# Performance work log

Measured on AMD Instinct MI355X. Metric: run time of the kernel, lower is better.

## Reference

```python
import jax, jax.numpy as jnp
import numpy as np

H, D = 8, 16
HID = H * D  # hidden_channels = 128
SQRT_D = float(np.sqrt(D))


def setup_inputs() -> dict:
    key = jax.random.key(0)
    ks = iter(jax.random.split(key, 64))
    def nrm(shape, scale):
        return jax.random.normal(next(ks), shape, dtype=jnp.float32) * scale
    def rint(n, hi):
        return jax.random.randint(next(ks), (n,), 0, hi, dtype=jnp.int32)
    E = 250000
    Nh, Ni, Nt = 8000, 40000, 20000
    inp = {
        'x_herb': nrm((Nh, 400), 1.0),
        'x_ing':  nrm((Ni, 300), 1.0),
        'x_tgt':  nrm((Nt, 200), 1.0),
        # per-type input projections
        'W_herb': nrm((400, HID), 0.05), 'b_herb': jnp.zeros((HID,), jnp.float32),
        'W_ing':  nrm((300, HID), 0.06), 'b_ing':  jnp.zeros((HID,), jnp.float32),
        'W_tgt':  nrm((200, HID), 0.07), 'b_tgt':  jnp.zeros((HID,), jnp.float32),
        # HGTConv per-node-type k/q/v linears, stacked over [herb, ing, tgt]
        'Wk': nrm((3, HID, HID), 0.09), 'bk': jnp.zeros((3, HID), jnp.float32),
        'Wq': nrm((3, HID, HID), 0.09), 'bq': jnp.zeros((3, HID), jnp.float32),
        'Wv': nrm((3, HID, HID), 0.09), 'bv': jnp.zeros((3, HID), jnp.float32),
        # per-edge-type relation matrices / priors, stacked over 4 edge types
        'a_rel': nrm((4, H, D, D), 0.25),
        'm_rel': nrm((4, H, D, D), 0.25),
        'p_rel': jnp.ones((4, H), jnp.float32),
        # per-dst-node-type output linear + skip gate
        'Wa': nrm((3, HID, HID), 0.09), 'ba': jnp.zeros((3, HID), jnp.float32),
        'skip': jnp.ones((3,), jnp.float32),
        # final herb linear
        'W_out': nrm((HID, HID), 0.09), 'b_out': jnp.zeros((HID,), jnp.float32),
        # edge lists: (herb->ing contains), (ing->herb rev), (ing->tgt targets), (tgt->ing rev)
        'src_ci': rint(E, Nh), 'dst_ci': rint(E, Ni),
        'src_ic': rint(E, Ni), 'dst_ic': rint(E, Nh),
        'src_it': rint(E, Ni), 'dst_it': rint(E, Nt),
        'src_ti': rint(E, Nt), 'dst_ti': rint(E, Ni),
    }
    return inp


def _hetero_forward(x_herb, x_ing, x_tgt, W_herb, b_herb, W_ing, b_ing, W_tgt, b_tgt,
                    Wk, bk, Wq, bq, Wv, bv, a_rel, m_rel, p_rel, Wa, ba, skip,
                    W_out, b_out, src_ci, dst_ci, src_ic, dst_ic, src_it, dst_it,
                    src_ti, dst_ti):
    types = ['herb', 'ing', 'tgt']
    xs = {'herb': x_herb @ W_herb + b_herb,
          'ing':  x_ing  @ W_ing  + b_ing,
          'tgt':  x_tgt  @ W_tgt  + b_tgt}
    Ns = {t: xs[t].shape[0] for t in types}
    # per-node-type k/q/v, reshaped to [N, H, D]
    k = {t: (xs[t] @ Wk[i] + bk[i]).reshape(-1, H, D) for i, t in enumerate(types)}
    q = {t: (xs[t] @ Wq[i] + bq[i]).reshape(-1, H, D) for i, t in enumerate(types)}
    v = {t: (xs[t] @ Wv[i] + bv[i]).reshape(-1, H, D) for i, t in enumerate(types)}

    edge_defs = [  # (edge_type_id, src_type, dst_type, src_idx, dst_idx)
        (0, 'herb', 'ing', src_ci, dst_ci),
        (1, 'ing', 'herb', src_ic, dst_ic),
        (2, 'ing', 'tgt', src_it, dst_it),
        (3, 'tgt', 'ing', src_ti, dst_ti),
    ]
    contrib = {t: [] for t in types}
    for e, s, t, src, dst in edge_defs:
        # relation-specific transforms at node level, then gather per edge
        k_rel = jnp.einsum('nhd,hde->nhe', k[s], a_rel[e])  # [Ns, H, D]
        v_rel = jnp.einsum('nhd,hde->nhe', v[s], m_rel[e])  # [Ns, H, D]
        logit = (q[t][dst] * k_rel[src]).sum(-1) * (p_rel[e] / SQRT_D)  # [E, H]
        contrib[t].append((logit, v_rel[src], dst))

    out = {}
    for i, t in enumerate(types):
        logits = jnp.concatenate([c[0] for c in contrib[t]], axis=0)  # [Et, H]
        msgs = jnp.concatenate([c[1] for c in contrib[t]], axis=0)    # [Et, H, D]
        dsts = jnp.concatenate([c[2] for c in contrib[t]], axis=0)    # [Et]
        n = Ns[t]
        # segment softmax over all incoming edges of each dst node (per head)
        mx = jax.ops.segment_max(logits, dsts, num_segments=n)
        ex = jnp.exp(logits - mx[dsts])
        den = jax.ops.segment_sum(ex, dsts, num_segments=n)
        alpha = ex / (den[dsts] + 1e-16)
        agg = jax.ops.segment_sum(msgs * alpha[:, :, None], dsts, num_segments=n)
        agg = agg.reshape(n, HID)
        o = jax.nn.gelu(agg, approximate=False) @ Wa[i] + ba[i]
        g = jax.nn.sigmoid(skip[i])
        out[t] = jax.nn.relu(g * o + (1.0 - g) * xs[t])
    out_herb = out['herb'] @ W_out + b_out
    return (out_herb, out['ing'], out['tgt'])


def reference(x_herb, x_ing, x_tgt, W_herb, b_herb, W_ing, b_ing, W_tgt, b_tgt,
              Wk, bk, Wq, bq, Wv, bv, a_rel, m_rel, p_rel, Wa, ba, skip,
              W_out, b_out, src_ci, dst_ci, src_ic, dst_ic, src_it, dst_it,
              src_ti, dst_ti):
    return _hetero_forward(x_herb, x_ing, x_tgt, W_herb, b_herb, W_ing, b_ing,
                           W_tgt, b_tgt, Wk, bk, Wq, bq, Wv, bv, a_rel, m_rel,
                           p_rel, Wa, ba, skip, W_out, b_out, src_ci, dst_ci,
                           src_ic, dst_ic, src_it, dst_it, src_ti, dst_ti)
```

## Files before the change

### kernel.cpp

```cpp
#include <hip/hip_runtime.h>
#include <math.h>

#define HID 128
typedef unsigned int uint;
typedef unsigned short ushort;
typedef __attribute__((ext_vector_type(8))) short short8;
typedef __attribute__((ext_vector_type(4))) float floatx4;
typedef __attribute__((ext_vector_type(2))) float f32x2;

__device__ __forceinline__ ushort f2b(float f) {
  uint u = __float_as_uint(f);
  u += 0x7fffu + ((u >> 16) & 1u);
  return (ushort)(u >> 16);
}
__device__ __forceinline__ float b2f(ushort s) {
  return __uint_as_float(((uint)s) << 16);
}
__device__ __forceinline__ float blo(uint u) { return __uint_as_float(u << 16); }
__device__ __forceinline__ float bhi(uint u) { return __uint_as_float(u & 0xffff0000u); }
__device__ __forceinline__ f32x2 b2x2(uint u) {
  f32x2 r;
  r.x = __uint_as_float(u << 16);
  r.y = __uint_as_float(u & 0xffff0000u);
  return r;
}

__device__ __forceinline__ void gll16(const ushort* g, ushort* l) {
  __builtin_amdgcn_global_load_lds(
      (const __attribute__((address_space(1))) void*)g,
      (__attribute__((address_space(3))) void*)l, 16, 0, 0);
}

__device__ __forceinline__ size_t a_packed_us(int rr, int col) {
  int tm = rr >> 7, prow = rr & 127;
  int ptk = col >> 5, kin = col & 31;
  int sw = (kin >> 3) ^ ((prow >> 1) & 3);
  return (((size_t)tm * 4 + ptk) * 512 + (size_t)prow * 4 + sw) * 8 + (kin & 7);
}

#define CSR_CH 2048
#define CSR_SH 9

struct EdgeStreams {
  const int* src[4]; const int* dst[4];
  int off[4]; uint rel[4]; uint ldb[4];
};

struct PackSeg { const float* X; ushort* out; int M, K, Ktiles, start; };
struct WBlk { const float* src; ushort* dst; int K; int start; };
struct Prolog {
  PackSeg pk[3];
  int crwstart, wstart, bstart, total;
  const float *Wk, *bk, *Wv, *bv, *a_rel, *m_rel, *p_rel;
  ushort* kw_dst[4];
  ushort* vw_dst[4];
  float* bcat;
  int kb_off[4], vb_off[4];
  WBlk wb[10];
  const float* bq;
  int bq_off[3];
  const int* edst[4];
  int eoff[4];
  uint* hist;
  int NBs, NBH, NBK, E;
};

__device__ void combine_rel_elem(const Prolog& P, int idx)
{
  int col  = idx & 127;
  int rest = idx >> 7;
  int row  = rest % 129;
  rest /= 129;
  int kv = rest & 1;
  int e  = rest >> 1;
  int i  = (e + 1) >> 1;
  int h = col >> 4, j = col & 15;
  const float* Wsrc = kv ? P.Wv : P.Wk;
  const float* bsrc = kv ? P.bv : P.bk;
  const float* rel  = kv ? P.m_rel : P.a_rel;
  float acc = 0.f;
  if (row < 128) {
#pragma unroll
    for (int d = 0; d < 16; ++d)
      acc += Wsrc[(size_t)i * 16384 + (size_t)row * 128 + h * 16 + d] *
             rel[((e * 8 + h) * 16 + d) * 16 + j];
  } else {
#pragma unroll
    for (int d = 0; d < 16; ++d)
      acc += bsrc[i * 128 + h * 16 + d] * rel[((e * 8 + h) * 16 + d) * 16 + j];
  }
  if (!kv) acc *= P.p_rel[e * 8 + h] * 0.36067376022224085f;
  if (row < 128) {
    ushort* dst = kv ? P.vw_dst[e] : P.kw_dst[e];
    int tk = row >> 5, chunk = (row >> 3) & 3, m = row & 7;
    int swf = chunk ^ ((col >> 1) & 3);
    dst[((tk * 512 + col * 4 + swf) << 3) + m] = f2b(acc);
  } else {
    P.bcat[(kv ? P.vb_off[e] : P.kb_off[e]) + col] = acc;
  }
}

__device__ void conv_elem(const Prolog& P, int s0)
{
  int si = 0;
#pragma unroll
  for (int k = 1; k < 10; ++k)
    if (s0 >= P.wb[k].start) si = k;
  WBlk b = P.wb[si];
  int s = s0 - b.start;
  int tk = s >> 9, o = s & 511;
  int c = o >> 2, swf = o & 3;
  int chunk = swf ^ ((c >> 1) & 3);
  int r0 = tk * 32 + chunk * 8;
  ushort tmp[8];
#pragma unroll
  for (int m = 0; m < 8; ++m) {
    int r = r0 + m;
    tmp[m] = (r < b.K) ? f2b(b.src[(size_t)r * 128 + c]) : (ushort)0;
  }
  *(short8*)&b.dst[(size_t)s * 8] = *(short8*)tmp;
}

__global__ __launch_bounds__(256)
void prologue(Prolog P)
{
  __shared__ uint h[512];
  int bI = blockIdx.x;
  if (bI < P.NBH) {
    int et = bI / P.NBs;
    int i0 = (bI - et * P.NBs) * CSR_CH;
    const int* dp = P.edst[et];
    int off = P.eoff[et];
    for (int t = threadIdx.x; t < P.NBK; t += 256) h[t] = 0;
    __syncthreads();
#pragma unroll
    for (int j = 0; j < CSR_CH / 256; ++j) {
      int idx = i0 + j * 256 + threadIdx.x;
      if (idx < P.E) atomicAdd(&h[(uint)(off + dp[idx]) >> CSR_SH], 1u);
    }
    __syncthreads();
    for (int t = threadIdx.x; t < P.NBK; t += 256)
      P.hist[(size_t)t * P.NBH + bI] = h[t];
    return;
  }
  int gtid = (bI - P.NBH) * 256 + threadIdx.x;
  if (gtid >= P.total) return;
  if (gtid >= P.bstart) {
    int j = gtid - P.bstart;
    P.bcat[P.bq_off[j >> 7] + (j & 127)] = P.bq[j];
    return;
  }
  if (gtid >= P.wstart) { conv_elem(P, gtid - P.wstart); return; }
  if (gtid >= P.crwstart) { combine_rel_elem(P, gtid - P.crwstart); return; }
  int si = 0;
  if (gtid >= P.pk[2].start) si = 2;
  else if (gtid >= P.pk[1].start) si = 1;
  const PackSeg s = P.pk[si];
  int slot = gtid - s.start;
  int spm = s.Ktiles << 9;
  int tm = slot / spm, r2 = slot - tm * spm;
  int tk = r2 >> 9, o = r2 & 511;
  int row = o >> 2, sw = o & 3;
  int chunk = sw ^ ((row >> 1) & 3);
  int grow = tm * 128 + row;
  int gk = tk * 32 + chunk * 8;
  ushort tmp[8];
  if (grow < s.M && gk + 8 <= s.K) {
    const float* p = s.X + (size_t)grow * s.K + gk;
    float4 a = *(const float4*)p, b = *(const float4*)(p + 4);
    tmp[0] = f2b(a.x); tmp[1] = f2b(a.y); tmp[2] = f2b(a.z); tmp[3] = f2b(a.w);
    tmp[4] = f2b(b.x); tmp[5] = f2b(b.y); tmp[6] = f2b(b.z); tmp[7] = f2b(b.w);
  } else {
#pragma unroll
    for (int j = 0; j < 8; ++j) {
      int kk = gk + j;
      tmp[j] = (grow < s.M && kk < s.K) ? f2b(s.X[(size_t)grow * s.K + kk]) : (ushort)0;
    }
  }
  *(short8*)&s.out[(size_t)slot * 8] = *(short8*)tmp;
}

__global__ __launch_bounds__(256)
void bucket_scan(uint* __restrict__ hist, uint* __restrict__ bucketTot, int NBH)
{
  __shared__ uint ws[4];
  __shared__ uint carry_s;
  int b = blockIdx.x;
  int t = threadIdx.x, lane = t & 63, w = t >> 6;
  if (t == 0) carry_s = 0;
  __syncthreads();
  for (int base = 0; base < NBH; base += 256) {
    int i = base + t;
    uint x = (i < NBH) ? hist[(size_t)b * NBH + i] : 0u;
    uint v = x;
#pragma unroll
    for (int o = 1; o < 64; o <<= 1) {
      uint y = __shfl_up(v, o, 64);
      if (lane >= o) v += y;
    }
    if (lane == 63) ws[w] = v;
    __syncthreads();
    uint add = carry_s;
    for (int k = 0; k < w; ++k) add += ws[k];
    if (i < NBH) hist[(size_t)b * NBH + i] = add + v - x;
    __syncthreads();
    if (t == 255) carry_s = add + v;
    __syncthreads();
  }
  if (t == 0) bucketTot[b] = carry_s;
}

__device__ __forceinline__ void base_scan(const uint* __restrict__ bucketTot,
                                          uint* sb, uint* ws, int NBK)
{
  int t = threadIdx.x, lane = t & 63, w = t >> 6;
  sb[t] = (t < NBK) ? bucketTot[t] : 0u;
  sb[t + 256] = (t + 256 < NBK) ? bucketTot[t + 256] : 0u;
  __syncthreads();
  uint a0 = sb[2 * t], a1 = sb[2 * t + 1];
  uint s = a0 + a1;
  uint v = s;
#pragma unroll
  for (int o = 1; o < 64; o <<= 1) {
    uint y = __shfl_up(v, o, 64);
    if (lane >= o) v += y;
  }
  if (lane == 63) ws[w] = v;
  __syncthreads();
  uint add = 0;
  for (int k = 0; k < w; ++k) add += ws[k];
  uint e0 = add + v - s;
  sb[2 * t] = e0;
  sb[2 * t + 1] = e0 + a0;
  __syncthreads();
}

__global__ __launch_bounds__(256)
void bucket_scatter(EdgeStreams es, const uint* __restrict__ hist,
                    const uint* __restrict__ bucketTot,
                    uint2* __restrict__ inter, int NBs, int NBH, int NBK, int E)
{
  __shared__ uint sb[516];
  __shared__ uint ws[4];
  __shared__ uint cur[512];
  base_scan(bucketTot, sb, ws, NBK);
  int b = blockIdx.x;
  int et = b / NBs;
  int i0 = (b - et * NBs) * CSR_CH;
  const int* dp = es.dst[et];
  const int* sp = es.src[et];
  int off = es.off[et];
  uint rel = es.rel[et], ldb = es.ldb[et];
  for (int t = threadIdx.x; t < NBK; t += 256)
    cur[t] = sb[t] + hist[(size_t)t * NBH + b];
  __syncthreads();
#pragma unroll
  for (int j = 0; j < CSR_CH / 256; ++j) {
    int idx = i0 + j * 256 + threadIdx.x;
    if (idx < E) {
      int g = off + dp[idx];
      uint pos = atomicAdd(&cur[(uint)g >> CSR_SH], 1u);
      inter[pos] = make_uint2(rel + (uint)sp[idx] * ldb, (uint)g);
    }
  }
}

__global__ __launch_bounds__(256)
void bucket_finalize(const uint2* __restrict__ inter,
                     const uint* __restrict__ bucketTot,
                     int* __restrict__ starts, uint* __restrict__ payload,
                     int Ntot, int NBK)
{
  __shared__ uint sb[516];
  __shared__ uint ncnt[512];
  __shared__ uint ws[4];
  base_scan(bucketTot, sb, ws, NBK);
  int b = blockIdx.x;
  int g0 = b << CSR_SH;
  int t = threadIdx.x, lane = t & 63, w = t >> 6;
  uint r0 = sb[b], r1 = sb[b + 1];
  if (b == NBK - 1 && t == 0) starts[Ntot] = (int)r1;
  ncnt[t] = 0; ncnt[t + 256] = 0;
  __syncthreads();
  for (uint i = r0 + t; i < r1; i += 256)
    atomicAdd(&ncnt[inter[i].y - g0], 1u);
  __syncthreads();
  uint a0 = ncnt[2 * t], a1 = ncnt[2 * t + 1];
  uint s = a0 + a1;
  uint v = s;
#pragma unroll
  for (int o = 1; o < 64; o <<= 1) {
    uint y = __shfl_up(v, o, 64);
    if (lane >= o) v += y;
  }
  if (lane == 63) ws[w] = v;
  __syncthreads();
  uint add = r0;
  for (int k = 0; k < w; ++k) add += ws[k];
  uint e0 = add + v - s;
  int gi = g0 + 2 * t;
  if (gi < Ntot)     starts[gi]     = (int)e0;
  if (gi + 1 < Ntot) starts[gi + 1] = (int)(e0 + a0);
  ncnt[2 * t] = e0;
  ncnt[2 * t + 1] = e0 + a0;
  __syncthreads();
  for (uint i = r0 + t; i < r1; i += 256) {
    uint2 rec = inter[i];
    uint pos = atomicAdd(&ncnt[rec.y - g0], 1u);
    payload[pos] = rec.x;
  }
}

struct GemmSeg {
  const ushort* A; const ushort* B; const float* bias;
  void* out; const ushort* xsP;
  int Ktiles, ldo, Mreal, skip_idx, epi, NT, start;
  int n2; const ushort* B2; const float* bias2;
  void* out2; int ldo2, Mreal2, epi2;
};
struct Gemm3 { GemmSeg s[3]; const float* skip; int nseg; };

__launch_bounds__(256)
__global__ void gemm_sched(Gemm3 g3)
{
  __shared__ __align__(16) ushort As[2][4096];
  __shared__ __align__(16) ushort Bs[2][4096];
  __shared__ __align__(16) ushort Xs[16384];
  int bid = blockIdx.x;
  int si = 0;
  if (g3.nseg > 1 && bid >= g3.s[1].start)
    si = (g3.nseg > 2 && bid >= g3.s[2].start) ? 2 : 1;
  const GemmSeg sg = g3.s[si];
  int local = bid - sg.start;
  int tm = local / sg.NT, tn = local - tm * sg.NT;

  const int t = threadIdx.x;
  const int wave = t >> 6, lane = t & 63;
  const int wm = (wave >> 1) * 64, wn = (wave & 1) * 64;
  const int l16 = lane & 15, quad = lane >> 4;
  const int Ktiles = sg.Ktiles;
  const int swz = (quad ^ ((l16 >> 1) & 3)) * 8;

  const ushort* Abase = sg.A + (size_t)tm * Ktiles * 4096;
  const ushort* Bbase = sg.B + (size_t)tn * Ktiles * 4096;

  floatx4 acc[4][4];
#pragma unroll
  for (int i = 0; i < 4; ++i)
#pragma unroll
    for (int j = 0; j < 4; ++j) acc[i][j] = (floatx4){0.f, 0.f, 0.f, 0.f};

  auto stage = [&](int tk, int buf) {
#pragma unroll
    for (int j = 0; j < 4; ++j) {
      int c = wave * 4 + j;
      if (c < 8)
        gll16(Abase + (size_t)tk * 4096 + c * 512 + lane * 8, &As[buf][c * 512]);
      else
        gll16(Bbase + (size_t)tk * 4096 + (c - 8) * 512 + lane * 8, &Bs[buf][(c - 8) * 512]);
    }
  };

  stage(0, 0);
  __syncthreads();

  for (int tk = 0; tk < Ktiles; ++tk) {
    int buf = tk & 1;
    if (tk + 1 < Ktiles) stage(tk + 1, buf ^ 1);

    short8 af[4], bfr[4];
#pragma unroll
    for (int i = 0; i < 4; ++i) {
      af[i]  = *(const short8*)&As[buf][(wm + i * 16 + l16) * 32 + swz];
      bfr[i] = *(const short8*)&Bs[buf][(wn + i * 16 + l16) * 32 + swz];
    }
#pragma unroll
    for (int mi = 0; mi < 4; ++mi)
#pragma unroll
      for (int ni = 0; ni < 4; ++ni)
        acc[mi][ni] = __builtin_amdgcn_mfma_f32_16x16x32_bf16(
            af[mi], bfr[ni], acc[mi][ni], 0, 0, 0);
    __syncthreads();
  }

  const int epi = sg.epi;
  float g = 0.f, omg = 0.f;
  if (epi == 2 || epi == 3 || epi == 5) {
    float s = g3.skip[sg.skip_idx];
    g = 1.f / (1.f + __expf(-s));
    omg = 1.f - g;
  }
#pragma unroll
  for (int ni = 0; ni < 4; ++ni) {
    int col = tn * 128 + wn + ni * 16 + l16;
    float bb = sg.bias[col];
    int ptk = col >> 5, kin = col & 31;
#pragma unroll
    for (int mi = 0; mi < 4; ++mi) {
      int rloc = wm + mi * 16 + quad * 4;
#pragma unroll
      for (int r = 0; r < 4; ++r) {
        int prow = rloc + r;
        int rr = tm * 128 + prow;
        float v = acc[mi][ni][r] + bb;
        if (epi == 0) {
          ((ushort*)sg.out)[(size_t)rr * sg.ldo + col] = f2b(v);
        } else if (epi == 1) {
          if (rr < sg.Mreal) ((float*)sg.out)[(size_t)rr * sg.ldo + col] = v;
        } else if (epi == 2) {
          if (rr < sg.Mreal) {
            float xo = b2f(sg.xsP[a_packed_us(rr, col)]);
            ((float*)sg.out)[(size_t)rr * sg.ldo + col] = fmaxf(g * v + omg * xo, 0.f);
          }
        } else if (epi == 3) {
          float xo = b2f(sg.xsP[a_packed_us(rr, col)]);
          ((ushort*)sg.out)[a_packed_us(rr, col)] = f2b(fmaxf(g * v + omg * xo, 0.f));
        } else if (epi == 4) {
          ushort bv = f2b(v);
          ((ushort*)sg.out)[a_packed_us(rr, col)] = bv;
          int sw2 = (kin >> 3) ^ ((prow >> 1) & 3);
          Xs[ptk * 4096 + prow * 32 + sw2 * 8 + (kin & 7)] = bv;
        } else {
          float xo = b2f(sg.xsP[a_packed_us(rr, col)]);
          int sw2 = (kin >> 3) ^ ((prow >> 1) & 3);
          Xs[ptk * 4096 + prow * 32 + sw2 * 8 + (kin & 7)] =
              f2b(fmaxf(g * v + omg * xo, 0.f));
        }
      }
    }
  }

  if (sg.n2 == 0) return;
  __syncthreads();
  for (int t2 = 0; t2 < sg.n2; ++t2) {
    const ushort* B2b = sg.B2 + (size_t)t2 * 16384;
    auto stage2 = [&](int tk, int buf) {
#pragma unroll
      for (int j = 0; j < 2; ++j) {
        int c = wave * 2 + j;
        gll16(B2b + (size_t)tk * 4096 + c * 512 + lane * 8, &Bs[buf][c * 512]);
      }
    };
    floatx4 a2[4][4];
#pragma unroll
    for (int i = 0; i < 4; ++i)
#pragma unroll
      for (int j = 0; j < 4; ++j) a2[i][j] = (floatx4){0.f, 0.f, 0.f, 0.f};
    stage2(0, 0);
    __syncthreads();
#pragma unroll
    for (int tk = 0; tk < 4; ++tk) {
      int buf = tk & 1;
      if (tk + 1 < 4) stage2(tk + 1, buf ^ 1);
      short8 af[4], bfr[4];
#pragma unroll
      for (int i = 0; i < 4; ++i) {
        af[i]  = *(const short8*)&Xs[tk * 4096 + (wm + i * 16 + l16) * 32 + swz];
        bfr[i] = *(const short8*)&Bs[buf][(wn + i * 16 + l16) * 32 + swz];
      }
#pragma unroll
      for (int mi = 0; mi < 4; ++mi)
#pragma unroll
        for (int ni = 0; ni < 4; ++ni)
          a2[mi][ni] = __builtin_amdgcn_mfma_f32_16x16x32_bf16(
              af[mi], bfr[ni], a2[mi][ni], 0, 0, 0);
      __syncthreads();
    }
#pragma unroll
    for (int ni = 0; ni < 4; ++ni) {
      int col = t2 * 128 + wn + ni * 16 + l16;
      float bb = sg.bias2[col];
#pragma unroll
      for (int mi = 0; mi < 4; ++mi) {
        int rloc = wm + mi * 16 + quad * 4;
#pragma unroll
        for (int r = 0; r < 4; ++r) {
          int rr = tm * 128 + rloc + r;
          float v = a2[mi][ni][r] + bb;
          if (sg.epi2 == 0) {
            ((ushort*)sg.out2)[(size_t)rr * sg.ldo2 + col] = f2b(v);
          } else {
            if (rr < sg.Mreal2) ((float*)sg.out2)[(size_t)rr * sg.ldo2 + col] = v;
          }
        }
      }
    }
  }
}

struct GatherType { const ushort* q; ushort* agg; int ldq; };
struct GatherDesc { GatherType ty[3]; int n0, n1; };

__launch_bounds__(256)
__global__ void gather_all(const int* __restrict__ starts,
                           const uint* __restrict__ payload,
                           const ushort* __restrict__ kvbase,
                           GatherDesc gd, int Ntot)
{
  int wid = (blockIdx.x * 256 + threadIdx.x) >> 6;
  if (wid >= Ntot) return;
  int lane = threadIdx.x & 63;
  int g = lane >> 4, l = lane & 15;

  GatherType T;
  int d;
  if (wid < gd.n0)      { T = gd.ty[0]; d = wid; }
  else if (wid < gd.n1) { T = gd.ty[1]; d = wid - gd.n0; }
  else                  { T = gd.ty[2]; d = wid - gd.n1; }

  const char* kvb = (const char*)kvbase;
  const uint lofs = (uint)l * 16u;

  uint4 qv = *(const uint4*)(T.q + (size_t)d * T.ldq + l * 8);
  f32x2 q0 = b2x2(qv.x), q1 = b2x2(qv.y), q2 = b2x2(qv.z), q3 = b2x2(qv.w);

  int e0 = starts[wid], e1 = starts[wid + 1];
  float lsum = 0.f;
  f32x2 ac0 = {0.f, 0.f}, ac1 = {0.f, 0.f}, ac2 = {0.f, 0.f}, ac3 = {0.f, 0.f};

  for (int eb = e0; eb < e1; eb += 8) {
    int eA = eb + g, eB = eA + 4;
    bool actA = eA < e1, actB = eB < e1;
    uint pA = payload[actA ? eA : e0];
    uint pB = payload[actB ? eB : e0];
    const char* bA = kvb + (pA + lofs);
    const char* bB = kvb + (pB + lofs);
    uint4 kA = *(const uint4*)bA;
    uint4 vA = *(const uint4*)(bA + 256);
    uint4 kB = *(const uint4*)bB;
    uint4 vB = *(const uint4*)(bB + 256);

    f32x2 dA = q0 * b2x2(kA.x);
    dA = __builtin_elementwise_fma(q1, b2x2(kA.y), dA);
    dA = __builtin_elementwise_fma(q2, b2x2(kA.z), dA);
    dA = __builtin_elementwise_fma(q3, b2x2(kA.w), dA);
    f32x2 dB = q0 * b2x2(kB.x);
    dB = __builtin_elementwise_fma(q1, b2x2(kB.y), dB);
    dB = __builtin_elementwise_fma(q2, b2x2(kB.z), dB);
    dB = __builtin_elementwise_fma(q3, b2x2(kB.w), dB);
    float pa = dA.x + dA.y;
    float pb = dB.x + dB.y;
    pa += __shfl_xor(pa, 1, 64);
    pb += __shfl_xor(pb, 1, 64);
    float exA = exp2f(fminf(pa, 115.4f));
    float exB = exp2f(fminf(pb, 115.4f));
    exA = actA ? exA : 0.f;
    exB = actB ? exB : 0.f;
    lsum += exA + exB;
    f32x2 xA = {exA, exA}, xB = {exB, exB};
    ac0 = __builtin_elementwise_fma(xA, b2x2(vA.x), ac0);
    ac1 = __builtin_elementwise_fma(xA, b2x2(vA.y), ac1);
    ac2 = __builtin_elementwise_fma(xA, b2x2(vA.z), ac2);
    ac3 = __builtin_elementwise_fma(xA, b2x2(vA.w), ac3);
    ac0 = __builtin_elementwise_fma(xB, b2x2(vB.x), ac0);
    ac1 = __builtin_elementwise_fma(xB, b2x2(vB.y), ac1);
    ac2 = __builtin_elementwise_fma(xB, b2x2(vB.z), ac2);
    ac3 = __builtin_elementwise_fma(xB, b2x2(vB.w), ac3);
  }

  float s0 = ac0.x, s1 = ac0.y, s2 = ac1.x, s3 = ac1.y;
  float s4 = ac2.x, s5 = ac2.y, s6 = ac3.x, s7 = ac3.y;
#define MRG(v) v += __shfl_xor(v, 16, 64); v += __shfl_xor(v, 32, 64)
  MRG(lsum); MRG(s0); MRG(s1); MRG(s2); MRG(s3); MRG(s4); MRG(s5); MRG(s6); MRG(s7);
#undef MRG

  float inv = 1.f / (lsum + 1e-16f);
  float m0 = (g & 1) ? s2 : s0, m1 = (g & 1) ? s6 : s4;
  float n0 = (g & 1) ? s3 : s1, n1 = (g & 1) ? s7 : s5;
  float x0 = ((g & 2) ? m1 : m0) * inv;
  float x1 = ((g & 2) ? n1 : n0) * inv;
  float g0 = 0.5f * x0 * (1.f + erff(x0 * 0.70710678118654752f));
  float g1 = 0.5f * x1 * (1.f + erff(x1 * 0.70710678118654752f));
  int tm = d >> 7, row = d & 127;
  int tk = l >> 2, sw = (l & 3) ^ ((row >> 1) & 3);
  size_t us = (((size_t)tm * 4 + tk) * 512 + (size_t)row * 4 + sw) * 8 + 2 * g;
  *(uint*)(T.agg + us) = ((uint)f2b(g1) << 16) | (uint)f2b(g0);
}

extern "C" void kernel_launch(void* const* d_in, const int* in_sizes, int n_in,
                              void* d_out, int out_size, void* d_ws, size_t ws_size,
                              hipStream_t stream)
{
  const float* x_herb = (const float*)d_in[0];
  const float* x_ing  = (const float*)d_in[1];
  const float* x_tgt  = (const float*)d_in[2];
  const float* W_herb = (const float*)d_in[3];
  const float* b_herb = (const float*)d_in[4];
  const float* W_ing  = (const float*)d_in[5];
  const float* b_ing  = (const float*)d_in[6];
  const float* W_tgt  = (const float*)d_in[7];
  const float* b_tgt  = (const float*)d_in[8];
  const float* Wk     = (const float*)d_in[9];
  const float* bk     = (const float*)d_in[10];
  const float* Wq     = (const float*)d_in[11];
  const float* bq     = (const float*)d_in[12];
  const float* Wv     = (const float*)d_in[13];
  const float* bv     = (const float*)d_in[14];
  const float* a_rel  = (const float*)d_in[15];
  const float* m_rel  = (const float*)d_in[16];
  const float* p_rel  = (const float*)d_in[17];
  const float* Wa     = (const float*)d_in[18];
  const float* ba     = (const float*)d_in[19];
  const float* skip   = (const float*)d_in[20];
  const float* W_out  = (const float*)d_in[21];
  const float* b_out  = (const float*)d_in[22];
  const int* srcs[4] = {(const int*)d_in[23], (const int*)d_in[25],
                        (const int*)d_in[27], (const int*)d_in[29]};
  const int* dsts[4] = {(const int*)d_in[24], (const int*)d_in[26],
                        (const int*)d_in[28], (const int*)d_in[30]};

  const int Nh = in_sizes[0] / 400;
  const int Ni = in_sizes[1] / 300;
  const int Nt = in_sizes[2] / 200;
  const int E  = in_sizes[23];
  const int Ntot = Nh + Ni + Nt;

  const int MT_h = (Nh + 127) / 128, MT_i = (Ni + 127) / 128, MT_t = (Nt + 127) / 128;
  const int KT_h = 13, KT_i = 10, KT_t = 7;

  const int NBs = (E + CSR_CH - 1) / CSR_CH;
  const int NBH = 4 * NBs;
  const int NBK = (Ntot + (1 << CSR_SH) - 1) >> CSR_SH;

  char* base = (char*)d_ws;
  size_t off = 0;
  auto A = [&](size_t bytes) -> void* {
    void* p = base + off; off += (bytes + 255) & ~(size_t)255; return p;
  };
  ushort* xp_h  = (ushort*)A((size_t)MT_h * KT_h * 8192);
  ushort* xp_i  = (ushort*)A((size_t)MT_i * KT_i * 8192);
  ushort* xp_t  = (ushort*)A((size_t)MT_t * KT_t * 8192);
  ushort* xsP_h = (ushort*)A((size_t)MT_h * 4 * 8192);
  ushort* xsP_i = (ushort*)A((size_t)MT_i * 4 * 8192);
  ushort* xsP_t = (ushort*)A((size_t)MT_t * 4 * 8192);
  ushort* fused_h = (ushort*)A((size_t)MT_h * 128 * 384 * 2);
  ushort* fused_i = (ushort*)A((size_t)MT_i * 128 * 640 * 2);
  ushort* fused_t = (ushort*)A((size_t)MT_t * 128 * 384 * 2);
  ushort* aggp_h  = (ushort*)A((size_t)MT_h * 4 * 8192);
  ushort* aggp_i  = (ushort*)A((size_t)MT_i * 4 * 8192);
  ushort* aggp_t  = (ushort*)A((size_t)MT_t * 4 * 8192);
  ushort* Weff1_h = (ushort*)A((size_t)KT_h * 8192);
  ushort* Weff1_i = (ushort*)A((size_t)KT_i * 8192);
  ushort* Weff1_t = (ushort*)A((size_t)KT_t * 8192);
  ushort* Wcat_h = (ushort*)A((size_t)3 * 4 * 8192);
  ushort* Wcat_i = (ushort*)A((size_t)5 * 4 * 8192);
  ushort* Wcat_t = (ushort*)A((size_t)3 * 4 * 8192);
  float* bcat   = (float*)A(1408 * 4);
  ushort* Wa_t   = (ushort*)A((size_t)3 * 16384 * 2);
  ushort* Wout_t = (ushort*)A((size_t)16384 * 2);
  int* starts  = (int*)A((size_t)(Ntot + 4) * 4);
  uint* payload = (uint*)A((size_t)(4 * E + 8) * 4);
  uint* hist    = (uint*)A((size_t)NBK * NBH * 4);
  uint* bucketTot  = (uint*)A((size_t)NBK * 4);
  uint2* inter  = (uint2*)A((size_t)(4 * E + 8) * 8);
  (void)ws_size; (void)n_in;

  const int toff_h = 0, toff_i = Nh, toff_t = Nh + Ni;
  dim3 blk(256);

  uint fi2 = (uint)((size_t)(fused_i - fused_h) * 2);
  uint ft2 = (uint)((size_t)(fused_t - fused_h) * 2);

  int sl_h = MT_h * KT_h * 512, sl_i = MT_i * KT_i * 512, sl_t = MT_t * KT_t * 512;
  Prolog P;
  P.pk[0] = {x_herb, xp_h, Nh, 400, KT_h, 0};
  P.pk[1] = {x_ing,  xp_i, Ni, 300, KT_i, sl_h};
  P.pk[2] = {x_tgt,  xp_t, Nt, 200, KT_t, sl_h + sl_i};
  P.crwstart = sl_h + sl_i + sl_t;
  P.wstart = P.crwstart + 4 * 2 * 129 * 128;
  {
    const float* wsrc10[10] = {W_herb, W_ing, W_tgt, Wq, Wq + 16384, Wq + 32768,
                               Wa, Wa + 16384, Wa + 32768, W_out};
    ushort* wdst10[10] = {Weff1_h, Weff1_i, Weff1_t, Wcat_h, Wcat_i, Wcat_t,
                          Wa_t, Wa_t + 16384, Wa_t + 32768, Wout_t};
    int wk10[10] = {400, 300, 200, 128, 128, 128, 128, 128, 128, 128};
    int wcum = 0;
    for (int z = 0; z < 10; ++z) {
      P.wb[z] = {wsrc10[z], wdst10[z], wk10[z], wcum};
      wcum += ((wk10[z] + 31) / 32) * 512;
    }
    P.bstart = P.wstart + wcum;
  }
  P.total = P.bstart + 384;
  P.Wk = Wk; P.bk = bk; P.Wv = Wv; P.bv = bv;
  P.a_rel = a_rel; P.m_rel = m_rel; P.p_rel = p_rel;
  P.kw_dst[0] = Wcat_h + 16384; P.vw_dst[0] = Wcat_h + 32768;
  P.kw_dst[1] = Wcat_i + 16384; P.vw_dst[1] = Wcat_i + 32768;
  P.kw_dst[2] = Wcat_i + 49152; P.vw_dst[2] = Wcat_i + 65536;
  P.kw_dst[3] = Wcat_t + 16384; P.vw_dst[3] = Wcat_t + 32768;
  P.bcat = bcat;
  P.kb_off[0] = 128;  P.vb_off[0] = 256;
  P.kb_off[1] = 512;  P.vb_off[1] = 640;
  P.kb_off[2] = 768;  P.vb_off[2] = 896;
  P.kb_off[3] = 1152; P.vb_off[3] = 1280;
  P.bq = bq;
  P.bq_off[0] = 0; P.bq_off[1] = 384; P.bq_off[2] = 1024;
  P.edst[0] = dsts[0]; P.eoff[0] = toff_i;
  P.edst[1] = dsts[1]; P.eoff[1] = toff_h;
  P.edst[2] = dsts[2]; P.eoff[2] = toff_t;
  P.edst[3] = dsts[3]; P.eoff[3] = toff_i;
  P.hist = hist; P.NBs = NBs; P.NBH = NBH; P.NBK = NBK; P.E = E;
  prologue<<<NBH + (P.total + 255) / 256, blk, 0, stream>>>(P);

  EdgeStreams ES;
  ES.src[0] = srcs[0]; ES.dst[0] = dsts[0]; ES.off[0] = toff_i;
  ES.rel[0] = 256u;        ES.ldb[0] = 768u;
  ES.src[1] = srcs[1]; ES.dst[1] = dsts[1]; ES.off[1] = toff_h;
  ES.rel[1] = fi2 + 256u;  ES.ldb[1] = 1280u;
  ES.src[2] = srcs[2]; ES.dst[2] = dsts[2]; ES.off[2] = toff_t;
  ES.rel[2] = fi2 + 768u;  ES.ldb[2] = 1280u;
  ES.src[3] = srcs[3]; ES.dst[3] = dsts[3]; ES.off[3] = toff_i;
  ES.rel[3] = ft2 + 256u;  ES.ldb[3] = 768u;
  bucket_scan<<<NBK, blk, 0, stream>>>(hist, bucketTot, NBH);
  bucket_scatter<<<NBH, blk, 0, stream>>>(ES, hist, bucketTot, inter, NBs, NBH, NBK, E);
  bucket_finalize<<<NBK, blk, 0, stream>>>(inter, bucketTot, starts, payload, Ntot, NBK);

  Gemm3 G1;
  G1.skip = skip; G1.nseg = 3;
  G1.s[0] = {xp_h, Weff1_h, b_herb, xsP_h, nullptr, KT_h, 0, 0, 0, 4, 1, 0,
             3, Wcat_h, bcat + 0, fused_h, 384, 0, 0};
  G1.s[1] = {xp_i, Weff1_i, b_ing,  xsP_i, nullptr, KT_i, 0, 0, 0, 4, 1, MT_h,
             5, Wcat_i, bcat + 384, fused_i, 640, 0, 0};
  G1.s[2] = {xp_t, Weff1_t, b_tgt,  xsP_t, nullptr, KT_t, 0, 0, 0, 4, 1, MT_h + MT_i,
             3, Wcat_t, bcat + 1024, fused_t, 384, 0, 0};
  gemm_sched<<<MT_h + MT_i + MT_t, blk, 0, stream>>>(G1);

  GatherDesc GD;
  GD.n0 = Nh; GD.n1 = Nh + Ni;
  GD.ty[0] = {fused_h, aggp_h, 384};
  GD.ty[1] = {fused_i, aggp_i, 640};
  GD.ty[2] = {fused_t, aggp_t, 384};
  gather_all<<<(Ntot + 3) / 4, blk, 0, stream>>>(starts, payload, fused_h, GD, Ntot);

  float* outp = (float*)d_out;
  float* out_herb = outp;
  float* out_ing  = outp + (size_t)Nh * HID;
  float* out_tgt  = outp + (size_t)(Nh + Ni) * HID;
  Gemm3 GE;
  GE.skip = skip; GE.nseg = 3;
  GE.s[0] = {aggp_h, Wa_t + 0 * 16384, ba + 0 * 128, nullptr, xsP_h,
             4, 0, 0, 0, 5, 1, 0,
             1, Wout_t, b_out, out_herb, 128, Nh, 1};
  GE.s[1] = {aggp_i, Wa_t + 1 * 16384, ba + 1 * 128, out_ing, xsP_i,
             4, 128, Ni, 1, 2, 1, MT_h,
             0, nullptr, nullptr, nullptr, 0, 0, 0};
  GE.s[2] = {aggp_t, Wa_t + 2 * 16384, ba + 2 * 128, out_tgt, xsP_t,
             4, 128, Nt, 2, 2, 1, MT_h + MT_i,
             0, nullptr, nullptr, nullptr, 0, 0, 0};
  gemm_sched<<<MT_h + MT_i + MT_t, blk, 0, stream>>>(GE);
  (void)out_size;
}
```

Measured before the change: 436.7 us.

## Alias GEMM LDS buffers, swap MFMA operands for vectorized epilogue stores

Merges the As/Bs/Xs shared arrays into a single aliased LDS region, cutting the GEMM kernel's shared memory footprint so more blocks can fit per CU. Swaps the MFMA operand order so each lane holds four consecutive output columns, which lets the epilogue use float4 bias loads and uint2/float4 vector stores in place of scalar stores. The second fused GEMM is restructured into a single continuous pipelined loop over all N2 tiles. Its first B2 tile is now prefetched before the first epilogue runs. Aliasing Xs onto the A/B staging buffers depends on correct barrier placement, and the prefetched B2 region must not overlap Xs.

Result: faster. 399.1 us (-8.6%).

```diff
diff --git a/kernel.cpp b/kernel.cpp
--- a/kernel.cpp
+++ b/kernel.cpp
@@ -323,9 +323,12 @@
 __launch_bounds__(256)
 __global__ void gemm_sched(Gemm3 g3)
 {
-  __shared__ __align__(16) ushort As[2][4096];
-  __shared__ __align__(16) ushort Bs[2][4096];
-  __shared__ __align__(16) ushort Xs[16384];
+  __shared__ __align__(16) ushort lds[24576];
+  ushort* As0 = lds;
+  ushort* Bs0 = lds + 8192;
+  ushort* Xs  = lds;
+  ushort* B2s = lds + 16384;
+
   int bid = blockIdx.x;
   int si = 0;
   if (g3.nseg > 1 && bid >= g3.s[1].start)
@@ -355,9 +358,17 @@
     for (int j = 0; j < 4; ++j) {
       int c = wave * 4 + j;
       if (c < 8)
-        gll16(Abase + (size_t)tk * 4096 + c * 512 + lane * 8, &As[buf][c * 512]);
+        gll16(Abase + (size_t)tk * 4096 + c * 512 + lane * 8, As0 + buf * 4096 + c * 512);
       else
-        gll16(Bbase + (size_t)tk * 4096 + (c - 8) * 512 + lane * 8, &Bs[buf][(c - 8) * 512]);
+        gll16(Bbase + (size_t)tk * 4096 + (c - 8) * 512 + lane * 8,
+              Bs0 + buf * 4096 + (c - 8) * 512);
+    }
+  };
+  auto stage2L = [&](int s2, int buf) {
+#pragma unroll
+    for (int j = 0; j < 2; ++j) {
+      int c = wave * 2 + j;
+      gll16(sg.B2 + (size_t)s2 * 4096 + c * 512 + lane * 8, B2s + buf * 4096 + c * 512);
     }
   };
 
@@ -371,17 +382,19 @@
     short8 af[4], bfr[4];
 #pragma unroll
     for (int i = 0; i < 4; ++i) {
-      af[i]  = *(const short8*)&As[buf][(wm + i * 16 + l16) * 32 + swz];
-      bfr[i] = *(const short8*)&Bs[buf][(wn + i * 16 + l16) * 32 + swz];
+      af[i]  = *(const short8*)&As0[buf * 4096 + (wm + i * 16 + l16) * 32 + swz];
+      bfr[i] = *(const short8*)&Bs0[buf * 4096 + (wn + i * 16 + l16) * 32 + swz];
     }
 #pragma unroll
     for (int mi = 0; mi < 4; ++mi)
 #pragma unroll
       for (int ni = 0; ni < 4; ++ni)
         acc[mi][ni] = __builtin_amdgcn_mfma_f32_16x16x32_bf16(
-            af[mi], bfr[ni], acc[mi][ni], 0, 0, 0);
+            bfr[ni], af[mi], acc[mi][ni], 0, 0, 0);
     __syncthreads();
   }
+
+  if (sg.n2 > 0) stage2L(0, 0);
 
   const int epi = sg.epi;
   float g = 0.f, omg = 0.f;
@@ -392,96 +405,110 @@
   }
 #pragma unroll
   for (int ni = 0; ni < 4; ++ni) {
-    int col = tn * 128 + wn + ni * 16 + l16;
-    float bb = sg.bias[col];
-    int ptk = col >> 5, kin = col & 31;
+    int cl = wn + ni * 16 + quad * 4;
+    int cb = tn * 128 + cl;
+    float4 b4 = *(const float4*)&sg.bias[cb];
 #pragma unroll
     for (int mi = 0; mi < 4; ++mi) {
-      int rloc = wm + mi * 16 + quad * 4;
-#pragma unroll
-      for (int r = 0; r < 4; ++r) {
-        int prow = rloc + r;
-        int rr = tm * 128 + prow;
-        float v = acc[mi][ni][r] + bb;
-        if (epi == 0) {
-          ((ushort*)sg.out)[(size_t)rr * sg.ldo + col] = f2b(v);
-        } else if (epi == 1) {
-          if (rr < sg.Mreal) ((float*)sg.out)[(size_t)rr * sg.ldo + col] = v;
-        } else if (epi == 2) {
-          if (rr < sg.Mreal) {
-            float xo = b2f(sg.xsP[a_packed_us(rr, col)]);
-            ((float*)sg.out)[(size_t)rr * sg.ldo + col] = fmaxf(g * v + omg * xo, 0.f);
+      int prow = wm + mi * 16 + l16;
+      int rr = tm * 128 + prow;
+      float v0 = acc[mi][ni][0] + b4.x;
+      float v1 = acc[mi][ni][1] + b4.y;
+      float v2 = acc[mi][ni][2] + b4.z;
+      float v3 = acc[mi][ni][3] + b4.w;
+      if (epi == 0) {
+        uint2 o = make_uint2(((uint)f2b(v1) << 16) | f2b(v0),
+                             ((uint)f2b(v3) << 16) | f2b(v2));
+        *(uint2*)&((ushort*)sg.out)[(size_t)rr * sg.ldo + cb] = o;
+      } else if (epi == 1) {
+        if (rr < sg.Mreal)
+          *(float4*)&((float*)sg.out)[(size_t)rr * sg.ldo + cb] =
+              make_float4(v0, v1, v2, v3);
+      } else if (epi == 2) {
+        if (rr < sg.Mreal) {
+          uint2 xo = *(const uint2*)&sg.xsP[a_packed_us(rr, cb)];
+          float4 o;
+          o.x = fmaxf(g * v0 + omg * blo(xo.x), 0.f);
+          o.y = fmaxf(g * v1 + omg * bhi(xo.x), 0.f);
+          o.z = fmaxf(g * v2 + omg * blo(xo.y), 0.f);
+          o.w = fmaxf(g * v3 + omg * bhi(xo.y), 0.f);
+          *(float4*)&((float*)sg.out)[(size_t)rr * sg.ldo + cb] = o;
+        }
+      } else if (epi == 3) {
+        uint2 xo = *(const uint2*)&sg.xsP[a_packed_us(rr, cb)];
+        uint2 o = make_uint2(
+            ((uint)f2b(fmaxf(g * v1 + omg * bhi(xo.x), 0.f)) << 16) |
+                   f2b(fmaxf(g * v0 + omg * blo(xo.x), 0.f)),
+            ((uint)f2b(fmaxf(g * v3 + omg * bhi(xo.y), 0.f)) << 16) |
+                   f2b(fmaxf(g * v2 + omg * blo(xo.y), 0.f)));
+        *(uint2*)&((ushort*)sg.out)[a_packed_us(rr, cb)] = o;
+      } else if (epi == 4) {
+        uint2 o = make_uint2(((uint)f2b(v1) << 16) | f2b(v0),
+                             ((uint)f2b(v3) << 16) | f2b(v2));
+        *(uint2*)&((ushort*)sg.out)[a_packed_us(rr, cb)] = o;
+        int sw2 = ((cl & 31) >> 3) ^ ((prow >> 1) & 3);
+        *(uint2*)&Xs[(cl >> 5) * 4096 + prow * 32 + sw2 * 8 + (cl & 7)] = o;
+      } else {
+        uint2 xo = *(const uint2*)&sg.xsP[a_packed_us(rr, cb)];
+        uint2 o = make_uint2(
+            ((uint)f2b(fmaxf(g * v1 + omg * bhi(xo.x), 0.f)) << 16) |
+                   f2b(fmaxf(g * v0 + omg * blo(xo.x), 0.f)),
+            ((uint)f2b(fmaxf(g * v3 + omg * bhi(xo.y), 0.f)) << 16) |
+                   f2b(fmaxf(g * v2 + omg * blo(xo.y), 0.f)));
+        int sw2 = ((cl & 31) >> 3) ^ ((prow >> 1) & 3);
+        *(uint2*)&Xs[(cl >> 5) * 4096 + prow * 32 + sw2 * 8 + (cl & 7)] = o;
+      }
+    }
+  }
+
+  if (sg.n2 == 0) return;
+  __syncthreads();
+  int total2 = sg.n2 * 4;
+  floatx4 a2[4][4];
+#pragma unroll
+  for (int i = 0; i < 4; ++i)
+#pragma unroll
+    for (int j = 0; j < 4; ++j) a2[i][j] = (floatx4){0.f, 0.f, 0.f, 0.f};
+  for (int s2 = 0; s2 < total2; ++s2) {
+    int buf = s2 & 1;
+    if (s2 + 1 < total2) stage2L(s2 + 1, buf ^ 1);
+    int xb = (s2 & 3) * 4096;
+    short8 af[4], bfr[4];
+#pragma unroll
+    for (int i = 0; i < 4; ++i) {
+      af[i]  = *(const short8*)&Xs[xb + (wm + i * 16 + l16) * 32 + swz];
+      bfr[i] = *(const short8*)&B2s[buf * 4096 + (wn + i * 16 + l16) * 32 + swz];
+    }
+#pragma unroll
+    for (int mi = 0; mi < 4; ++mi)
+#pragma unroll
+      for (int ni = 0; ni < 4; ++ni)
+        a2[mi][ni] = __builtin_amdgcn_mfma_f32_16x16x32_bf16(
+            bfr[ni], af[mi], a2[mi][ni], 0, 0, 0);
+    __syncthreads();
+    if ((s2 & 3) == 3) {
+      int t2 = s2 >> 2;
+#pragma unroll
+      for (int ni = 0; ni < 4; ++ni) {
+        int cb2 = t2 * 128 + wn + ni * 16 + quad * 4;
+        float4 b4 = *(const float4*)&sg.bias2[cb2];
+#pragma unroll
+        for (int mi = 0; mi < 4; ++mi) {
+          int rr = tm * 128 + wm + mi * 16 + l16;
+          float v0 = a2[mi][ni][0] + b4.x;
+          float v1 = a2[mi][ni][1] + b4.y;
+          float v2 = a2[mi][ni][2] + b4.z;
+          float v3 = a2[mi][ni][3] + b4.w;
+          if (sg.epi2 == 0) {
+            uint2 o = make_uint2(((uint)f2b(v1) << 16) | f2b(v0),
+                                 ((uint)f2b(v3) << 16) | f2b(v2));
+            *(uint2*)&((ushort*)sg.out2)[(size_t)rr * sg.ldo2 + cb2] = o;
+          } else {
+            if (rr < sg.Mreal2)
+              *(float4*)&((float*)sg.out2)[(size_t)rr * sg.ldo2 + cb2] =
+                  make_float4(v0, v1, v2, v3);
           }
-        } else if (epi == 3) {
-          float xo = b2f(sg.xsP[a_packed_us(rr, col)]);
-          ((ushort*)sg.out)[a_packed_us(rr, col)] = f2b(fmaxf(g * v + omg * xo, 0.f));
-        } else if (epi == 4) {
-          ushort bv = f2b(v);
-          ((ushort*)sg.out)[a_packed_us(rr, col)] = bv;
-          int sw2 = (kin >> 3) ^ ((prow >> 1) & 3);
-          Xs[ptk * 4096 + prow * 32 + sw2 * 8 + (kin & 7)] = bv;
-        } else {
-          float xo = b2f(sg.xsP[a_packed_us(rr, col)]);
-          int sw2 = (kin >> 3) ^ ((prow >> 1) & 3);
-          Xs[ptk * 4096 + prow * 32 + sw2 * 8 + (kin & 7)] =
-              f2b(fmaxf(g * v + omg * xo, 0.f));
-        }
-      }
-    }
-  }
-
-  if (sg.n2 == 0) return;
-  __syncthreads();
-  for (int t2 = 0; t2 < sg.n2; ++t2) {
-    const ushort* B2b = sg.B2 + (size_t)t2 * 16384;
-    auto stage2 = [&](int tk, int buf) {
-#pragma unroll
-      for (int j = 0; j < 2; ++j) {
-        int c = wave * 2 + j;
-        gll16(B2b + (size_t)tk * 4096 + c * 512 + lane * 8, &Bs[buf][c * 512]);
-      }
-    };
-    floatx4 a2[4][4];
-#pragma unroll
-    for (int i = 0; i < 4; ++i)
-#pragma unroll
-      for (int j = 0; j < 4; ++j) a2[i][j] = (floatx4){0.f, 0.f, 0.f, 0.f};
-    stage2(0, 0);
-    __syncthreads();
-#pragma unroll
-    for (int tk = 0; tk < 4; ++tk) {
-      int buf = tk & 1;
-      if (tk + 1 < 4) stage2(tk + 1, buf ^ 1);
-      short8 af[4], bfr[4];
-#pragma unroll
-      for (int i = 0; i < 4; ++i) {
-        af[i]  = *(const short8*)&Xs[tk * 4096 + (wm + i * 16 + l16) * 32 + swz];
-        bfr[i] = *(const short8*)&Bs[buf][(wn + i * 16 + l16) * 32 + swz];
-      }
-#pragma unroll
-      for (int mi = 0; mi < 4; ++mi)
-#pragma unroll
-        for (int ni = 0; ni < 4; ++ni)
-          a2[mi][ni] = __builtin_amdgcn_mfma_f32_16x16x32_bf16(
-              af[mi], bfr[ni], a2[mi][ni], 0, 0, 0);
-      __syncthreads();
-    }
-#pragma unroll
-    for (int ni = 0; ni < 4; ++ni) {
-      int col = t2 * 128 + wn + ni * 16 + l16;
-      float bb = sg.bias2[col];
-#pragma unroll
-      for (int mi = 0; mi < 4; ++mi) {
-        int rloc = wm + mi * 16 + quad * 4;
-#pragma unroll
-        for (int r = 0; r < 4; ++r) {
-          int rr = tm * 128 + rloc + r;
-          float v = a2[mi][ni][r] + bb;
-          if (sg.epi2 == 0) {
-            ((ushort*)sg.out2)[(size_t)rr * sg.ldo2 + col] = f2b(v);
-          } else {
-            if (rr < sg.Mreal2) ((float*)sg.out2)[(size_t)rr * sg.ldo2 + col] = v;
-          }
+          a2[mi][ni] = (floatx4){0.f, 0.f, 0.f, 0.f};
         }
       }
     }
```
